# Kernel optimization log

Measured on AMD Instinct MI355X. Metric: run time of the kernel, lower is better.

## Reference

```python
import jax, jax.numpy as jnp
import numpy as np

BN_EPS = 1e-5
DIST_EPS = 1e-8


def setup_inputs() -> dict:
    key = jax.random.key(0)
    ks = jax.random.split(key, 8)
    B, N, M = 8, 8192, 2048
    C1, C2 = 128, 256
    Cin = C1 + C2  # 384
    H = 256
    return {
        "xyz1": jax.random.normal(ks[0], (B, N, 3), dtype=jnp.float32),
        "xyz2": jax.random.normal(ks[1], (B, M, 3), dtype=jnp.float32),
        "points1": jax.random.normal(ks[2], (B, N, C1), dtype=jnp.float32),
        "points2": jax.random.normal(ks[3], (B, M, C2), dtype=jnp.float32),
        "W1": jax.random.normal(ks[4], (H, Cin), dtype=jnp.float32) * 0.05,
        "b1": jnp.zeros((H,), dtype=jnp.float32),
        "gamma1": jnp.ones((H,), dtype=jnp.float32),
        "beta1": jnp.zeros((H,), dtype=jnp.float32),
        "W2": jax.random.normal(ks[5], (H, H), dtype=jnp.float32) * 0.05,
        "b2": jnp.zeros((H,), dtype=jnp.float32),
        "gamma2": jnp.ones((H,), dtype=jnp.float32),
        "beta2": jnp.zeros((H,), dtype=jnp.float32),
    }


def _interpolate(xyz1, xyz2, points2):
    # squared distances (B,N,M) via the bmm expansion, as in square_distance
    d = (jnp.sum(xyz1 * xyz1, -1)[:, :, None]
         + jnp.sum(xyz2 * xyz2, -1)[:, None, :]
         - 2.0 * jnp.einsum("bnc,bmc->bnm", xyz1, xyz2))
    neg, idx = jax.lax.top_k(-d, 3)          # 3 smallest distances
    dists = -neg                              # (B,N,3)
    recip = 1.0 / (dists + DIST_EPS)
    w = recip / jnp.sum(recip, -1, keepdims=True)  # (B,N,3)
    gathered = jax.vmap(lambda p, i: p[i])(points2, idx)  # (B,N,3,C2)
    return jnp.einsum("bnkc,bnk->bnc", gathered, w)


def _conv_bn_relu(x, W, b, gamma, beta):
    # pointwise conv1d: (B,N,Cin) x (Cout,Cin) -> (B,N,Cout)
    y = jnp.einsum("bnc,oc->bno", x, W) + b
    mean = jnp.mean(y, axis=(0, 1))           # BatchNorm1d (training-mode batch stats)
    var = jnp.var(y, axis=(0, 1))
    y = (y - mean) * jax.lax.rsqrt(var + BN_EPS) * gamma + beta
    return jax.nn.relu(y)


def reference(xyz1, xyz2, points1, points2, W1, b1, gamma1, beta1, W2, b2, gamma2, beta2):
    interp = _interpolate(xyz1, xyz2, points2)          # (B,N,C2)
    x = jnp.concatenate([points1, interp], axis=-1)     # (B,N,C1+C2)
    x = _conv_bn_relu(x, W1, b1, gamma1, beta1)
    x = _conv_bn_relu(x, W2, b2, gamma2, beta2)
    return x  # (B,N,mlp[-1])
```

## Files before the change

### kernel.cpp

```cpp
#include <hip/hip_runtime.h>
#include <hip/hip_bf16.h>
#include <stdint.h>

#define B_SZ  8
#define N_Q   8192
#define M_PT  2048
#define C1    128
#define C2    256
#define CIN   384
#define H_OUT 256
#define R_TOT 65536

#define NCH   8
#define CHM   (M_PT / NCH)
#define QPB   32

typedef __bf16 bf16x8 __attribute__((ext_vector_type(8)));
typedef __bf16 bf16x4 __attribute__((ext_vector_type(4)));
typedef __bf16 bf16x2 __attribute__((ext_vector_type(2)));
typedef float  f32x4  __attribute__((ext_vector_type(4)));

__device__ __forceinline__ void async_copy16(const void* g, void* l) {
    __builtin_amdgcn_global_load_lds(
        (const __attribute__((address_space(1))) unsigned int*)g,
        (__attribute__((address_space(3))) unsigned int*)l,
        16, 0, 0);
}

__global__ __launch_bounds__(256) void knn_vals(
    const float* __restrict__ xyz1, const float* __restrict__ xyz2,
    float4* __restrict__ vals4) {
    __shared__ float4 pos[CHM];
    const int tid = threadIdx.x;
    const int c   = blockIdx.x & (NCH - 1);
    const int qb  = (blockIdx.x >> 3) & 31;
    const int b   = blockIdx.x >> 8;
    {
        const float* x2 = xyz2 + ((size_t)b * M_PT + c * CHM) * 3;
        float x = x2[tid * 3], y = x2[tid * 3 + 1], z = x2[tid * 3 + 2];
        pos[tid] = make_float4(-2.f * x, -2.f * y, -2.f * z,
                               fmaf(x, x, fmaf(y, y, z * z)));
    }
    __syncthreads();

    const int q = b * N_Q + qb * 256 + tid;
    const float* q1 = xyz1 + (size_t)q * 3;
    float x1 = q1[0], y1 = q1[1], z1 = q1[2];
    float v0 = 3.4e38f, v1 = 3.4e38f, v2 = 3.4e38f;
#pragma unroll 8
    for (int j = 0; j < CHM; ++j) {
        float4 p = pos[j];
        float d  = fmaf(p.x, x1, fmaf(p.y, y1, fmaf(p.z, z1, p.w)));
        float n0 = fminf(d, v0);
        float n1 = __builtin_amdgcn_fmed3f(d, v0, v1);
        float n2 = __builtin_amdgcn_fmed3f(d, v1, v2);
        v0 = n0; v1 = n1; v2 = n2;
    }
    vals4[(size_t)c * R_TOT + q] = make_float4(v0, v1, v2, 0.f);
}

__global__ __launch_bounds__(256) void knn_merge(
    const float4* __restrict__ vals4, const float* __restrict__ xyz1,
    const float* __restrict__ W1,     const float* __restrict__ W2,
    __bf16* __restrict__ wb1,         __bf16* __restrict__ wb2,
    float4* __restrict__ v4,          float4* __restrict__ w4) {
    const int q = blockIdx.x * 256 + threadIdx.x;

    wb1[q] = (__bf16)W1[q];
    if (q < H_OUT * CIN - R_TOT) wb1[R_TOT + q] = (__bf16)W1[R_TOT + q];
    wb2[q] = (__bf16)W2[q];

    float v0 = 3.4e38f, v1 = 3.4e38f, v2 = 3.4e38f;
#pragma unroll
    for (int c = 0; c < NCH; ++c) {
        float4 t = vals4[(size_t)c * R_TOT + q];
#pragma unroll
        for (int k = 0; k < 3; ++k) {
            float d  = (k == 0) ? t.x : (k == 1) ? t.y : t.z;
            float n0 = fminf(d, v0);
            float n1 = __builtin_amdgcn_fmed3f(d, v0, v1);
            float n2 = __builtin_amdgcn_fmed3f(d, v1, v2);
            v0 = n0; v1 = n1; v2 = n2;
        }
    }
    const float* q1 = xyz1 + (size_t)q * 3;
    float x1 = q1[0], y1 = q1[1], z1 = q1[2];
    float n1q = fmaf(x1, x1, fmaf(y1, y1, z1 * z1));
    float r0 = 1.f / ((v0 + n1q) + 1e-8f);
    float r1 = 1.f / ((v1 + n1q) + 1e-8f);
    float r2 = 1.f / ((v2 + n1q) + 1e-8f);
    float rs = 1.f / (r0 + r1 + r2);
    v4[q] = make_float4(v0, v1, v2, 0.f);
    w4[q] = make_float4(r0 * rs, r1 * rs, r2 * rs, 0.f);
}

__global__ __launch_bounds__(256) void knn_recover(
    const float* __restrict__ xyz1, const float* __restrict__ xyz2,
    const float4* __restrict__ v4, int4* __restrict__ ci4) {
    __shared__ float4 pos[CHM];
    const int tid = threadIdx.x;
    const int c   = blockIdx.x & (NCH - 1);
    const int qb  = (blockIdx.x >> 3) & 31;
    const int b   = blockIdx.x >> 8;
    {
        const float* x2 = xyz2 + ((size_t)b * M_PT + c * CHM) * 3;
        float x = x2[tid * 3], y = x2[tid * 3 + 1], z = x2[tid * 3 + 2];
        pos[tid] = make_float4(-2.f * x, -2.f * y, -2.f * z,
                               fmaf(x, x, fmaf(y, y, z * z)));
    }
    __syncthreads();

    const int q = b * N_Q + qb * 256 + tid;
    const float* q1 = xyz1 + (size_t)q * 3;
    float x1 = q1[0], y1 = q1[1], z1 = q1[2];
    const float4 vv = v4[q];
    int i0 = 0x7fffffff, i1 = 0x7fffffff, i2 = 0x7fffffff;
    const int jb = c * CHM;
#pragma unroll 4
    for (int j = 0; j < CHM; ++j) {
        float4 p = pos[j];
        float d  = fmaf(p.x, x1, fmaf(p.y, y1, fmaf(p.z, z1, p.w)));
        if (d <= vv.z) {
            const int jj = jb + j;
            i0 = min(i0, (d == vv.x) ? jj : 0x7fffffff);
            i1 = min(i1, (d == vv.y) ? jj : 0x7fffffff);
            i2 = min(i2, (d == vv.z) ? jj : 0x7fffffff);
        }
    }
    ci4[(size_t)c * R_TOT + q] = make_int4(i0, i1, i2, 0);
}

__global__ __launch_bounds__(256) void interp_gather(
    const float* __restrict__ p1,  const float* __restrict__ p2,
    const int4* __restrict__ ci4,  const float4* __restrict__ w4,
    __bf16* __restrict__ xb) {
    __shared__ float wgt[QPB * 3];
    __shared__ int   ids[QPB * 3];

    const int tid = threadIdx.x;
    const int b   = blockIdx.x >> 8;
    const int q0  = (blockIdx.x & 255) * QPB;

    if (tid < QPB) {
        const int q = b * N_Q + q0 + tid;
        int i0 = 0x7fffffff, i1 = 0x7fffffff, i2 = 0x7fffffff;
#pragma unroll
        for (int c = 0; c < NCH; ++c) {
            int4 t = ci4[(size_t)c * R_TOT + q];
            i0 = min(i0, t.x); i1 = min(i1, t.y); i2 = min(i2, t.z);
        }
        float4 w = w4[q];
        wgt[tid * 3] = w.x; wgt[tid * 3 + 1] = w.y; wgt[tid * 3 + 2] = w.z;
        ids[tid * 3] = i0;  ids[tid * 3 + 1] = i1;  ids[tid * 3 + 2] = i2;
    }
    __syncthreads();

    const int wave = tid >> 6, lane = tid & 63;
    const float* p2b = p2 + (size_t)b * M_PT * C2;
    const float* p1b = p1 + (size_t)(b * N_Q + q0) * C1;
    __bf16* outp = xb + (size_t)(b * N_Q + q0) * CIN;
    for (int qq = wave; qq < QPB; qq += 4) {
        float w0 = wgt[qq * 3], w1 = wgt[qq * 3 + 1], w2 = wgt[qq * 3 + 2];
        int   j0 = ids[qq * 3], j1 = ids[qq * 3 + 1], j2 = ids[qq * 3 + 2];
        const float4* ra = (const float4*)(p2b + (size_t)j0 * C2);
        const float4* rb = (const float4*)(p2b + (size_t)j1 * C2);
        const float4* rc = (const float4*)(p2b + (size_t)j2 * C2);
        float4 va = ra[lane], vb = rb[lane], vc = rc[lane];
        bf16x4 o;
        o[0] = (__bf16)(w0 * va.x + w1 * vb.x + w2 * vc.x);
        o[1] = (__bf16)(w0 * va.y + w1 * vb.y + w2 * vc.y);
        o[2] = (__bf16)(w0 * va.z + w1 * vb.z + w2 * vc.z);
        o[3] = (__bf16)(w0 * va.w + w1 * vb.w + w2 * vc.w);
        *(bf16x4*)(outp + (size_t)qq * CIN + C1 + lane * 4) = o;
        float2 pv = ((const float2*)(p1b + (size_t)qq * C1))[lane];
        bf16x2 o2; o2[0] = (__bf16)pv.x; o2[1] = (__bf16)pv.y;
        *(bf16x2*)(outp + (size_t)qq * CIN + lane * 2) = o2;
    }
}

template <int K>
__global__ __launch_bounds__(256, 2) void gemm_bt(const __bf16* __restrict__ A,
                                                  const __bf16* __restrict__ Bw,
                                                  __bf16* __restrict__ Cout,
                                                  float* __restrict__ partS,
                                                  float* __restrict__ partQ) {
    __shared__ __attribute__((aligned(16))) __bf16 As[128 * 32];
    __shared__ __attribute__((aligned(16))) __bf16 Bs[128 * 32];
    const int tid  = threadIdx.x;
    const int wave = tid >> 6, lane = tid & 63;
    const int wm = wave >> 1, wn = wave & 1;
    const int quad = lane >> 4, r16 = lane & 15;
    const int bx = blockIdx.x & 1, by = blockIdx.x >> 1;
    const int l4 = lane >> 2, lk = (lane & 3) * 8;

    f32x4 acc[4][4] = {};

    const __bf16* gA = A  + (size_t)(by * 128 + wave * 32 + l4) * K + lk;
    const __bf16* gB = Bw + (size_t)(bx * 128 + wave * 32 + l4) * K + lk;
    char* lA = (char*)As + wave * 2048;
    char* lB = (char*)Bs + wave * 2048;

    for (int k0 = 0; k0 < K; k0 += 32) {
        async_copy16(gA + k0,                  lA);
        async_copy16(gA + k0 + (size_t)16 * K, lA + 1024);
        async_copy16(gB + k0,                  lB);
        async_copy16(gB + k0 + (size_t)16 * K, lB + 1024);
        __syncthreads();

        bf16x8 af[4], bf[4];
#pragma unroll
        for (int t = 0; t < 4; ++t)
            af[t] = *(const bf16x8*)(As + (wm * 64 + t * 16 + r16) * 32 + quad * 8);
#pragma unroll
        for (int u = 0; u < 4; ++u)
            bf[u] = *(const bf16x8*)(Bs + (wn * 64 + u * 16 + r16) * 32 + quad * 8);
#pragma unroll
        for (int t = 0; t < 4; ++t)
#pragma unroll
            for (int u = 0; u < 4; ++u)
                acc[t][u] = __builtin_amdgcn_mfma_f32_16x16x32_bf16(af[t], bf[u], acc[t][u], 0, 0, 0);
        __syncthreads();
    }

#pragma unroll
    for (int t = 0; t < 4; ++t) {
#pragma unroll
        for (int u = 0; u < 4; ++u) {
            const int col = bx * 128 + wn * 64 + u * 16 + r16;
#pragma unroll
            for (int r = 0; r < 4; ++r) {
                const int row = by * 128 + wm * 64 + t * 16 + quad * 4 + r;
                Cout[(size_t)row * H_OUT + col] = (__bf16)acc[t][u][r];
            }
        }
    }

    float* redS = (float*)As;
    float* redQ = ((float*)As) + 1024;
    const int slot = wm * 4 + quad;
#pragma unroll
    for (int u = 0; u < 4; ++u) {
        float s = 0.f, qq = 0.f;
#pragma unroll
        for (int t = 0; t < 4; ++t)
#pragma unroll
            for (int r = 0; r < 4; ++r) { float v = acc[t][u][r]; s += v; qq = fmaf(v, v, qq); }
        const int col = wn * 64 + u * 16 + r16;
        redS[col * 8 + slot] = s;
        redQ[col * 8 + slot] = qq;
    }
    __syncthreads();
    if (tid < 128) {
        float s = 0.f, qq = 0.f;
#pragma unroll
        for (int k = 0; k < 8; ++k) { s += redS[tid * 8 + k]; qq += redQ[tid * 8 + k]; }
        partS[(size_t)blockIdx.x * 128 + tid] = s;
        partQ[(size_t)blockIdx.x * 128 + tid] = qq;
    }
}

__global__ __launch_bounds__(256) void bn_finalize(const float* __restrict__ pS,
                                                   const float* __restrict__ pQ,
                                                   const float* __restrict__ gamma,
                                                   const float* __restrict__ beta,
                                                   float* __restrict__ sc,
                                                   float* __restrict__ sh) {
    __shared__ float rs[256], rq[256];
    const int c = blockIdx.x;
    const int t = threadIdx.x;
    const int half = c >> 7, lo = c & 127;
    const size_t o1 = (size_t)(2 * t + half) * 128 + lo;
    const size_t o2 = (size_t)(2 * (t + 256) + half) * 128 + lo;
    rs[t] = pS[o1] + pS[o2];
    rq[t] = pQ[o1] + pQ[o2];
    __syncthreads();
    for (int k = 128; k > 0; k >>= 1) {
        if (t < k) { rs[t] += rs[t + k]; rq[t] += rq[t + k]; }
        __syncthreads();
    }
    if (t == 0) {
        const float inv = 1.f / (float)R_TOT;
        float mean = rs[0] * inv;
        float var  = rq[0] * inv - mean * mean;
        float a    = gamma[c] * rsqrtf(var + 1e-5f);
        sc[c] = a;
        sh[c] = beta[c] - mean * a;
    }
}

__global__ __launch_bounds__(256) void apply_bf16(__bf16* __restrict__ y,
                                                  const float* __restrict__ sc,
                                                  const float* __restrict__ sh) {
    __shared__ float scs[256], shs[256];
    scs[threadIdx.x] = sc[threadIdx.x];
    shs[threadIdx.x] = sh[threadIdx.x];
    __syncthreads();
    size_t i = ((size_t)blockIdx.x * 256 + threadIdx.x) * 8;
    int c0 = (int)(i & 255);
    bf16x8 v = *(const bf16x8*)(y + i);
#pragma unroll
    for (int e = 0; e < 8; ++e) {
        float f = fmaf((float)v[e], scs[c0 + e], shs[c0 + e]);
        v[e] = (__bf16)fmaxf(f, 0.f);
    }
    *(bf16x8*)(y + i) = v;
}

__global__ __launch_bounds__(256) void apply_out(const __bf16* __restrict__ y,
                                                 const float* __restrict__ sc,
                                                 const float* __restrict__ sh,
                                                 float* __restrict__ out) {
    __shared__ float scs[256], shs[256];
    scs[threadIdx.x] = sc[threadIdx.x];
    shs[threadIdx.x] = sh[threadIdx.x];
    __syncthreads();
    size_t i = ((size_t)blockIdx.x * 256 + threadIdx.x) * 8;
    int c0 = (int)(i & 255);
    bf16x8 v = *(const bf16x8*)(y + i);
    f32x4 o0, o1;
#pragma unroll
    for (int e = 0; e < 4; ++e)
        o0[e] = fmaxf(fmaf((float)v[e], scs[c0 + e], shs[c0 + e]), 0.f);
#pragma unroll
    for (int e = 0; e < 4; ++e)
        o1[e] = fmaxf(fmaf((float)v[4 + e], scs[c0 + 4 + e], shs[c0 + 4 + e]), 0.f);
    *(f32x4*)(out + i)     = o0;
    *(f32x4*)(out + i + 4) = o1;
}

extern "C" void kernel_launch(void* const* d_in, const int* in_sizes, int n_in,
                              void* d_out, int out_size, void* d_ws, size_t ws_size,
                              hipStream_t stream) {
    const float* xyz1 = (const float*)d_in[0];
    const float* xyz2 = (const float*)d_in[1];
    const float* p1   = (const float*)d_in[2];
    const float* p2   = (const float*)d_in[3];
    const float* W1   = (const float*)d_in[4];
    const float* g1   = (const float*)d_in[6];
    const float* be1  = (const float*)d_in[7];
    const float* W2   = (const float*)d_in[8];
    const float* g2   = (const float*)d_in[10];
    const float* be2  = (const float*)d_in[11];
    float* out = (float*)d_out;

    char* ws = (char*)d_ws;
    __bf16* xb     = (__bf16*)(ws);
    __bf16* y1b    = (__bf16*)(ws + 50331648);
    float4* vals4  = (float4*)(ws + 50331648);
    int4*   ci4    = (int4*)  (ws + 58720256);
    float4* v4     = (float4*)(ws + 67108864);
    float4* w4     = (float4*)(ws + 68157440);
    __bf16* y2b    = (__bf16*)(ws);
    float*  partS2 = (float*) (ws + 35651584);
    float*  partQ2 = partS2 + 131072;
    __bf16* wb1    = (__bf16*)(ws + 83886080);
    __bf16* wb2    = (__bf16*)(ws + 84082688);
    float*  sc1    = (float*) (ws + 84213760);
    float*  sh1    = sc1 + 256;
    float*  sc2    = sc1 + 512;
    float*  sh2    = sc1 + 768;

    float* partS1 = (float*)d_out;
    float* partQ1 = partS1 + 131072;

    knn_vals<<<B_SZ * 32 * NCH, 256, 0, stream>>>(xyz1, xyz2, vals4);
    knn_merge<<<R_TOT / 256, 256, 0, stream>>>(vals4, xyz1, W1, W2, wb1, wb2, v4, w4);
    knn_recover<<<B_SZ * 32 * NCH, 256, 0, stream>>>(xyz1, xyz2, v4, ci4);
    interp_gather<<<R_TOT / QPB, 256, 0, stream>>>(p1, p2, ci4, w4, xb);

    gemm_bt<CIN><<<1024, 256, 0, stream>>>(xb, wb1, y1b, partS1, partQ1);
    bn_finalize<<<256, 256, 0, stream>>>(partS1, partQ1, g1, be1, sc1, sh1);
    apply_bf16<<<8192, 256, 0, stream>>>(y1b, sc1, sh1);

    gemm_bt<H_OUT><<<1024, 256, 0, stream>>>(y1b, wb2, y2b, partS2, partQ2);
    bn_finalize<<<256, 256, 0, stream>>>(partS2, partQ2, g2, be2, sc2, sh2);
    apply_out<<<8192, 256, 0, stream>>>(y2b, sc2, sh2, out);
}
```

Before: 274.9 us.

## Project points2 through W1 before interpolation and fuse gather into first GEMM

Uses linearity to compute points2·W1b^T once per source point (2048 rows per batch instead of 8192 queries), then gathers and blends the three projected rows in the epilogue of a K=128 GEMM over points1. The concat buffer, the separate interp_gather kernel and the knn_merge kernel are removed. Merging moves into knn_recover, and the bf16 conversions of weights and inputs are folded into the kNN kernels. The change shrinks the first GEMM's work and the intermediate memory traffic. In exchange it adds scattered bf16 gathers in the epilogue and a different rounding order, since the projection is rounded to bf16 before blending.

Measured after the change: 261.7 us. -4.8%, faster.

```diff
diff --git a/kernel.cpp b/kernel.cpp
--- a/kernel.cpp
+++ b/kernel.cpp
@@ -13,11 +13,9 @@
 
 #define NCH   8
 #define CHM   (M_PT / NCH)
-#define QPB   32
 
 typedef __bf16 bf16x8 __attribute__((ext_vector_type(8)));
 typedef __bf16 bf16x4 __attribute__((ext_vector_type(4)));
-typedef __bf16 bf16x2 __attribute__((ext_vector_type(2)));
 typedef float  f32x4  __attribute__((ext_vector_type(4)));
 
 __device__ __forceinline__ void async_copy16(const void* g, void* l) {
@@ -29,12 +27,37 @@
 
 __global__ __launch_bounds__(256) void knn_vals(
     const float* __restrict__ xyz1, const float* __restrict__ xyz2,
+    const float* __restrict__ p2,   const float* __restrict__ W1,
+    const float* __restrict__ W2,
+    __bf16* __restrict__ p2b,  __bf16* __restrict__ wb1a,
+    __bf16* __restrict__ wb1b, __bf16* __restrict__ wb2,
     float4* __restrict__ vals4) {
     __shared__ float4 pos[CHM];
     const int tid = threadIdx.x;
     const int c   = blockIdx.x & (NCH - 1);
     const int qb  = (blockIdx.x >> 3) & 31;
     const int b   = blockIdx.x >> 8;
+    const int gid = blockIdx.x * 256 + tid;
+
+    {
+        const float4* src = (const float4*)p2 + (size_t)gid * 2;
+        float4 a = src[0], bb = src[1];
+        bf16x8 o;
+        o[0]=(__bf16)a.x; o[1]=(__bf16)a.y; o[2]=(__bf16)a.z; o[3]=(__bf16)a.w;
+        o[4]=(__bf16)bb.x; o[5]=(__bf16)bb.y; o[6]=(__bf16)bb.z; o[7]=(__bf16)bb.w;
+        *(bf16x8*)(p2b + (size_t)gid * 8) = o;
+    }
+    if (blockIdx.x < 384) {
+        const int e = gid;
+        const int o = e / 384, k = e - o * 384;
+        __bf16 v = (__bf16)W1[e];
+        if (k < C1) wb1a[o * C1 + k] = v;
+        else        wb1b[o * C2 + (k - C1)] = v;
+    } else if (blockIdx.x < 640) {
+        const int e = gid - 98304;
+        wb2[e] = (__bf16)W2[e];
+    }
+
     {
         const float* x2 = xyz2 + ((size_t)b * M_PT + c * CHM) * 3;
         float x = x2[tid * 3], y = x2[tid * 3 + 1], z = x2[tid * 3 + 2];
@@ -59,21 +82,46 @@
     vals4[(size_t)c * R_TOT + q] = make_float4(v0, v1, v2, 0.f);
 }
 
-__global__ __launch_bounds__(256) void knn_merge(
-    const float4* __restrict__ vals4, const float* __restrict__ xyz1,
-    const float* __restrict__ W1,     const float* __restrict__ W2,
-    __bf16* __restrict__ wb1,         __bf16* __restrict__ wb2,
-    float4* __restrict__ v4,          float4* __restrict__ w4) {
-    const int q = blockIdx.x * 256 + threadIdx.x;
-
-    wb1[q] = (__bf16)W1[q];
-    if (q < H_OUT * CIN - R_TOT) wb1[R_TOT + q] = (__bf16)W1[R_TOT + q];
-    wb2[q] = (__bf16)W2[q];
+__global__ __launch_bounds__(256) void knn_recover(
+    const float* __restrict__ xyz1, const float* __restrict__ xyz2,
+    const float* __restrict__ p1,   const float4* __restrict__ vals4,
+    __bf16* __restrict__ p1b, float4* __restrict__ w4,
+    int4* __restrict__ ci4) {
+    __shared__ float4 pos[CHM];
+    const int tid = threadIdx.x;
+    const int c   = blockIdx.x & (NCH - 1);
+    const int qb  = (blockIdx.x >> 3) & 31;
+    const int b   = blockIdx.x >> 8;
+    const int gid = blockIdx.x * 256 + tid;
+
+    {
+        const float4* src = (const float4*)p1 + (size_t)gid * 4;
+        float4 a = src[0], bb = src[1], cc = src[2], dd = src[3];
+        bf16x8 o0, o1;
+        o0[0]=(__bf16)a.x; o0[1]=(__bf16)a.y; o0[2]=(__bf16)a.z; o0[3]=(__bf16)a.w;
+        o0[4]=(__bf16)bb.x; o0[5]=(__bf16)bb.y; o0[6]=(__bf16)bb.z; o0[7]=(__bf16)bb.w;
+        o1[0]=(__bf16)cc.x; o1[1]=(__bf16)cc.y; o1[2]=(__bf16)cc.z; o1[3]=(__bf16)cc.w;
+        o1[4]=(__bf16)dd.x; o1[5]=(__bf16)dd.y; o1[6]=(__bf16)dd.z; o1[7]=(__bf16)dd.w;
+        *(bf16x8*)(p1b + (size_t)gid * 16)     = o0;
+        *(bf16x8*)(p1b + (size_t)gid * 16 + 8) = o1;
+    }
+
+    {
+        const float* x2 = xyz2 + ((size_t)b * M_PT + c * CHM) * 3;
+        float x = x2[tid * 3], y = x2[tid * 3 + 1], z = x2[tid * 3 + 2];
+        pos[tid] = make_float4(-2.f * x, -2.f * y, -2.f * z,
+                               fmaf(x, x, fmaf(y, y, z * z)));
+    }
+    __syncthreads();
+
+    const int q = b * N_Q + qb * 256 + tid;
+    const float* q1 = xyz1 + (size_t)q * 3;
+    float x1 = q1[0], y1 = q1[1], z1 = q1[2];
 
     float v0 = 3.4e38f, v1 = 3.4e38f, v2 = 3.4e38f;
 #pragma unroll
-    for (int c = 0; c < NCH; ++c) {
-        float4 t = vals4[(size_t)c * R_TOT + q];
+    for (int cc = 0; cc < NCH; ++cc) {
+        float4 t = vals4[(size_t)cc * R_TOT + q];
 #pragma unroll
         for (int k = 0; k < 3; ++k) {
             float d  = (k == 0) ? t.x : (k == 1) ? t.y : t.z;
@@ -83,102 +131,32 @@
             v0 = n0; v1 = n1; v2 = n2;
         }
     }
-    const float* q1 = xyz1 + (size_t)q * 3;
-    float x1 = q1[0], y1 = q1[1], z1 = q1[2];
-    float n1q = fmaf(x1, x1, fmaf(y1, y1, z1 * z1));
-    float r0 = 1.f / ((v0 + n1q) + 1e-8f);
-    float r1 = 1.f / ((v1 + n1q) + 1e-8f);
-    float r2 = 1.f / ((v2 + n1q) + 1e-8f);
-    float rs = 1.f / (r0 + r1 + r2);
-    v4[q] = make_float4(v0, v1, v2, 0.f);
-    w4[q] = make_float4(r0 * rs, r1 * rs, r2 * rs, 0.f);
-}
-
-__global__ __launch_bounds__(256) void knn_recover(
-    const float* __restrict__ xyz1, const float* __restrict__ xyz2,
-    const float4* __restrict__ v4, int4* __restrict__ ci4) {
-    __shared__ float4 pos[CHM];
-    const int tid = threadIdx.x;
-    const int c   = blockIdx.x & (NCH - 1);
-    const int qb  = (blockIdx.x >> 3) & 31;
-    const int b   = blockIdx.x >> 8;
-    {
-        const float* x2 = xyz2 + ((size_t)b * M_PT + c * CHM) * 3;
-        float x = x2[tid * 3], y = x2[tid * 3 + 1], z = x2[tid * 3 + 2];
-        pos[tid] = make_float4(-2.f * x, -2.f * y, -2.f * z,
-                               fmaf(x, x, fmaf(y, y, z * z)));
-    }
-    __syncthreads();
-
-    const int q = b * N_Q + qb * 256 + tid;
-    const float* q1 = xyz1 + (size_t)q * 3;
-    float x1 = q1[0], y1 = q1[1], z1 = q1[2];
-    const float4 vv = v4[q];
+    if (c == 0) {
+        float n1q = fmaf(x1, x1, fmaf(y1, y1, z1 * z1));
+        float r0 = 1.f / ((v0 + n1q) + 1e-8f);
+        float r1 = 1.f / ((v1 + n1q) + 1e-8f);
+        float r2 = 1.f / ((v2 + n1q) + 1e-8f);
+        float rs = 1.f / (r0 + r1 + r2);
+        w4[q] = make_float4(r0 * rs, r1 * rs, r2 * rs, 0.f);
+    }
+
     int i0 = 0x7fffffff, i1 = 0x7fffffff, i2 = 0x7fffffff;
     const int jb = c * CHM;
 #pragma unroll 4
     for (int j = 0; j < CHM; ++j) {
         float4 p = pos[j];
         float d  = fmaf(p.x, x1, fmaf(p.y, y1, fmaf(p.z, z1, p.w)));
-        if (d <= vv.z) {
+        if (d <= v2) {
             const int jj = jb + j;
-            i0 = min(i0, (d == vv.x) ? jj : 0x7fffffff);
-            i1 = min(i1, (d == vv.y) ? jj : 0x7fffffff);
-            i2 = min(i2, (d == vv.z) ? jj : 0x7fffffff);
+            i0 = min(i0, (d == v0) ? jj : 0x7fffffff);
+            i1 = min(i1, (d == v1) ? jj : 0x7fffffff);
+            i2 = min(i2, (d == v2) ? jj : 0x7fffffff);
         }
     }
     ci4[(size_t)c * R_TOT + q] = make_int4(i0, i1, i2, 0);
 }
 
-__global__ __launch_bounds__(256) void interp_gather(
-    const float* __restrict__ p1,  const float* __restrict__ p2,
-    const int4* __restrict__ ci4,  const float4* __restrict__ w4,
-    __bf16* __restrict__ xb) {
-    __shared__ float wgt[QPB * 3];
-    __shared__ int   ids[QPB * 3];
-
-    const int tid = threadIdx.x;
-    const int b   = blockIdx.x >> 8;
-    const int q0  = (blockIdx.x & 255) * QPB;
-
-    if (tid < QPB) {
-        const int q = b * N_Q + q0 + tid;
-        int i0 = 0x7fffffff, i1 = 0x7fffffff, i2 = 0x7fffffff;
-#pragma unroll
-        for (int c = 0; c < NCH; ++c) {
-            int4 t = ci4[(size_t)c * R_TOT + q];
-            i0 = min(i0, t.x); i1 = min(i1, t.y); i2 = min(i2, t.z);
-        }
-        float4 w = w4[q];
-        wgt[tid * 3] = w.x; wgt[tid * 3 + 1] = w.y; wgt[tid * 3 + 2] = w.z;
-        ids[tid * 3] = i0;  ids[tid * 3 + 1] = i1;  ids[tid * 3 + 2] = i2;
-    }
-    __syncthreads();
-
-    const int wave = tid >> 6, lane = tid & 63;
-    const float* p2b = p2 + (size_t)b * M_PT * C2;
-    const float* p1b = p1 + (size_t)(b * N_Q + q0) * C1;
-    __bf16* outp = xb + (size_t)(b * N_Q + q0) * CIN;
-    for (int qq = wave; qq < QPB; qq += 4) {
-        float w0 = wgt[qq * 3], w1 = wgt[qq * 3 + 1], w2 = wgt[qq * 3 + 2];
-        int   j0 = ids[qq * 3], j1 = ids[qq * 3 + 1], j2 = ids[qq * 3 + 2];
-        const float4* ra = (const float4*)(p2b + (size_t)j0 * C2);
-        const float4* rb = (const float4*)(p2b + (size_t)j1 * C2);
-        const float4* rc = (const float4*)(p2b + (size_t)j2 * C2);
-        float4 va = ra[lane], vb = rb[lane], vc = rc[lane];
-        bf16x4 o;
-        o[0] = (__bf16)(w0 * va.x + w1 * vb.x + w2 * vc.x);
-        o[1] = (__bf16)(w0 * va.y + w1 * vb.y + w2 * vc.y);
-        o[2] = (__bf16)(w0 * va.z + w1 * vb.z + w2 * vc.z);
-        o[3] = (__bf16)(w0 * va.w + w1 * vb.w + w2 * vc.w);
-        *(bf16x4*)(outp + (size_t)qq * CIN + C1 + lane * 4) = o;
-        float2 pv = ((const float2*)(p1b + (size_t)qq * C1))[lane];
-        bf16x2 o2; o2[0] = (__bf16)pv.x; o2[1] = (__bf16)pv.y;
-        *(bf16x2*)(outp + (size_t)qq * CIN + lane * 2) = o2;
-    }
-}
-
-template <int K>
+template <int K, bool STATS>
 __global__ __launch_bounds__(256, 2) void gemm_bt(const __bf16* __restrict__ A,
                                                   const __bf16* __restrict__ Bw,
                                                   __bf16* __restrict__ Cout,
@@ -235,6 +213,124 @@
         }
     }
 
+    if constexpr (STATS) {
+        float* redS = (float*)As;
+        float* redQ = ((float*)As) + 1024;
+        const int slot = wm * 4 + quad;
+#pragma unroll
+        for (int u = 0; u < 4; ++u) {
+            float s = 0.f, qq = 0.f;
+#pragma unroll
+            for (int t = 0; t < 4; ++t)
+#pragma unroll
+                for (int r = 0; r < 4; ++r) { float v = acc[t][u][r]; s += v; qq = fmaf(v, v, qq); }
+            const int col = wn * 64 + u * 16 + r16;
+            redS[col * 8 + slot] = s;
+            redQ[col * 8 + slot] = qq;
+        }
+        __syncthreads();
+        if (tid < 128) {
+            float s = 0.f, qq = 0.f;
+#pragma unroll
+            for (int k = 0; k < 8; ++k) { s += redS[tid * 8 + k]; qq += redQ[tid * 8 + k]; }
+            partS[(size_t)blockIdx.x * 128 + tid] = s;
+            partQ[(size_t)blockIdx.x * 128 + tid] = qq;
+        }
+    }
+}
+
+__global__ __launch_bounds__(256, 2) void gemm_a_int(
+    const __bf16* __restrict__ A,  const __bf16* __restrict__ Bw,
+    const __bf16* __restrict__ zb, const int4* __restrict__ ci4,
+    const float4* __restrict__ w4, __bf16* __restrict__ Cout,
+    float* __restrict__ partS, float* __restrict__ partQ) {
+    constexpr int K = C1;
+    __shared__ __attribute__((aligned(16))) __bf16 As[128 * 32];
+    __shared__ __attribute__((aligned(16))) __bf16 Bs[128 * 32];
+    const int tid  = threadIdx.x;
+    const int wave = tid >> 6, lane = tid & 63;
+    const int wm = wave >> 1, wn = wave & 1;
+    const int quad = lane >> 4, r16 = lane & 15;
+    const int bx = blockIdx.x & 1, by = blockIdx.x >> 1;
+    const int l4 = lane >> 2, lk = (lane & 3) * 8;
+
+    f32x4 acc[4][4] = {};
+
+    const __bf16* gA = A  + (size_t)(by * 128 + wave * 32 + l4) * K + lk;
+    const __bf16* gB = Bw + (size_t)(bx * 128 + wave * 32 + l4) * K + lk;
+    char* lA = (char*)As + wave * 2048;
+    char* lB = (char*)Bs + wave * 2048;
+
+    for (int k0 = 0; k0 < K; k0 += 32) {
+        async_copy16(gA + k0,                  lA);
+        async_copy16(gA + k0 + (size_t)16 * K, lA + 1024);
+        async_copy16(gB + k0,                  lB);
+        async_copy16(gB + k0 + (size_t)16 * K, lB + 1024);
+        __syncthreads();
+
+        bf16x8 af[4], bf[4];
+#pragma unroll
+        for (int t = 0; t < 4; ++t)
+            af[t] = *(const bf16x8*)(As + (wm * 64 + t * 16 + r16) * 32 + quad * 8);
+#pragma unroll
+        for (int u = 0; u < 4; ++u)
+            bf[u] = *(const bf16x8*)(Bs + (wn * 64 + u * 16 + r16) * 32 + quad * 8);
+#pragma unroll
+        for (int t = 0; t < 4; ++t)
+#pragma unroll
+            for (int u = 0; u < 4; ++u)
+                acc[t][u] = __builtin_amdgcn_mfma_f32_16x16x32_bf16(af[t], bf[u], acc[t][u], 0, 0, 0);
+        __syncthreads();
+    }
+
+    if (tid < 128) {
+        const int q = by * 128 + tid;
+        int i0 = 0x7fffffff, i1 = 0x7fffffff, i2 = 0x7fffffff;
+#pragma unroll
+        for (int cc = 0; cc < NCH; ++cc) {
+            int4 t4 = ci4[(size_t)cc * R_TOT + q];
+            i0 = min(i0, t4.x); i1 = min(i1, t4.y); i2 = min(i2, t4.z);
+        }
+        float4 w = w4[q];
+        ((int4*)As)[tid * 2]       = make_int4(i0, i1, i2, 0);
+        ((float4*)As)[tid * 2 + 1] = make_float4(w.x, w.y, w.z, 0.f);
+    }
+    __syncthreads();
+
+    const int bbase = (by >> 6) * M_PT;
+#pragma unroll
+    for (int t = 0; t < 4; ++t) {
+#pragma unroll
+        for (int r = 0; r < 4; ++r) {
+            const int rl = wm * 64 + t * 16 + quad * 4 + r;
+            const int4   ii = ((const int4*)As)[rl * 2];
+            const float4 ww = ((const float4*)As)[rl * 2 + 1];
+            const __bf16* z0 = zb + (size_t)(bbase + ii.x) * H_OUT;
+            const __bf16* z1 = zb + (size_t)(bbase + ii.y) * H_OUT;
+            const __bf16* z2 = zb + (size_t)(bbase + ii.z) * H_OUT;
+#pragma unroll
+            for (int u = 0; u < 4; ++u) {
+                const int col = bx * 128 + wn * 64 + u * 16 + r16;
+                acc[t][u][r] += ww.x * (float)z0[col] + ww.y * (float)z1[col]
+                              + ww.z * (float)z2[col];
+            }
+        }
+    }
+
+#pragma unroll
+    for (int t = 0; t < 4; ++t) {
+#pragma unroll
+        for (int u = 0; u < 4; ++u) {
+            const int col = bx * 128 + wn * 64 + u * 16 + r16;
+#pragma unroll
+            for (int r = 0; r < 4; ++r) {
+                const int row = by * 128 + wm * 64 + t * 16 + quad * 4 + r;
+                Cout[(size_t)row * H_OUT + col] = (__bf16)acc[t][u][r];
+            }
+        }
+    }
+
+    __syncthreads();
     float* redS = (float*)As;
     float* redQ = ((float*)As) + 1024;
     const int slot = wm * 4 + quad;
@@ -344,35 +440,38 @@
     float* out = (float*)d_out;
 
     char* ws = (char*)d_ws;
-    __bf16* xb     = (__bf16*)(ws);
-    __bf16* y1b    = (__bf16*)(ws + 50331648);
-    float4* vals4  = (float4*)(ws + 50331648);
-    int4*   ci4    = (int4*)  (ws + 58720256);
-    float4* v4     = (float4*)(ws + 67108864);
-    float4* w4     = (float4*)(ws + 68157440);
-    __bf16* y2b    = (__bf16*)(ws);
-    float*  partS2 = (float*) (ws + 35651584);
-    float*  partQ2 = partS2 + 131072;
-    __bf16* wb1    = (__bf16*)(ws + 83886080);
-    __bf16* wb2    = (__bf16*)(ws + 84082688);
-    float*  sc1    = (float*) (ws + 84213760);
-    float*  sh1    = sc1 + 256;
-    float*  sc2    = sc1 + 512;
-    float*  sh2    = sc1 + 768;
+    __bf16* y1b   = (__bf16*)(ws);
+    int4*   ci4   = (int4*)  (ws + 33554432);
+    float4* vals4 = (float4*)(ws + 41943040);
+    __bf16* zb    = (__bf16*)(ws + 41943040);
+    float4* w4    = (float4*)(ws + 50331648);
+    __bf16* p2b   = (__bf16*)(ws + 51380224);
+    __bf16* p1b   = (__bf16*)(ws + 59768832);
+    __bf16* y2b   = (__bf16*)(ws + 33554432);
+    __bf16* wb1a  = (__bf16*)(ws + 76546048);
+    __bf16* wb1b  = (__bf16*)(ws + 76611584);
+    __bf16* wb2   = (__bf16*)(ws + 76742656);
+    float*  sc1   = (float*) (ws + 76873728);
+    float*  sh1   = sc1 + 256;
+    float*  sc2   = sc1 + 512;
+    float*  sh2   = sc1 + 768;
 
     float* partS1 = (float*)d_out;
     float* partQ1 = partS1 + 131072;
-
-    knn_vals<<<B_SZ * 32 * NCH, 256, 0, stream>>>(xyz1, xyz2, vals4);
-    knn_merge<<<R_TOT / 256, 256, 0, stream>>>(vals4, xyz1, W1, W2, wb1, wb2, v4, w4);
-    knn_recover<<<B_SZ * 32 * NCH, 256, 0, stream>>>(xyz1, xyz2, v4, ci4);
-    interp_gather<<<R_TOT / QPB, 256, 0, stream>>>(p1, p2, ci4, w4, xb);
-
-    gemm_bt<CIN><<<1024, 256, 0, stream>>>(xb, wb1, y1b, partS1, partQ1);
+    float* partS2 = partS1 + 262144;
+    float* partQ2 = partS1 + 393216;
+
+    knn_vals<<<2048, 256, 0, stream>>>(xyz1, xyz2, p2, W1, W2,
+                                       p2b, wb1a, wb1b, wb2, vals4);
+    knn_recover<<<2048, 256, 0, stream>>>(xyz1, xyz2, p1, vals4, p1b, w4, ci4);
+
+    gemm_bt<C2, false><<<256, 256, 0, stream>>>(p2b, wb1b, zb, nullptr, nullptr);
+    gemm_a_int<<<1024, 256, 0, stream>>>(p1b, wb1a, zb, ci4, w4, y1b,
+                                         partS1, partQ1);
     bn_finalize<<<256, 256, 0, stream>>>(partS1, partQ1, g1, be1, sc1, sh1);
     apply_bf16<<<8192, 256, 0, stream>>>(y1b, sc1, sh1);
 
-    gemm_bt<H_OUT><<<1024, 256, 0, stream>>>(y1b, wb2, y2b, partS2, partQ2);
+    gemm_bt<H_OUT, true><<<1024, 256, 0, stream>>>(y1b, wb2, y2b, partS2, partQ2);
     bn_finalize<<<256, 256, 0, stream>>>(partS2, partQ2, g2, be2, sc2, sh2);
     apply_out<<<8192, 256, 0, stream>>>(y2b, sc2, sh2, out);
 }
```
